# Kernel tuning notes

Measured on AMD Instinct MI355X. Metric: run time of the kernel, lower is better.

## Reference

```python
import jax, jax.numpy as jnp
import numpy as np

B, S, C, M, L = 32, 8192, 64, 16, 4  # batch, seq, n_enc, n_modes, n_layers


def setup_inputs() -> dict:
    key = jax.random.key(0)
    ks = jax.random.split(key, 12)
    scale = 1.0 / (C * M)
    return {
        "input_tensor": jax.random.normal(ks[0], (B, S, 1), dtype=jnp.float32),
        "enc_w": jax.random.normal(ks[1], (C, 1), dtype=jnp.float32) * 0.1,
        "enc_b": jax.random.normal(ks[2], (C,), dtype=jnp.float32) * 0.1,
        "R_re": jax.random.normal(ks[3], (L, C, C, M), dtype=jnp.float32) * scale,
        "R_im": jax.random.normal(ks[4], (L, C, C, M), dtype=jnp.float32) * scale,
        "Wl_w": jax.random.normal(ks[5], (L, C, C), dtype=jnp.float32) * 0.1,
        "Wl_b": jax.random.normal(ks[6], (L, C), dtype=jnp.float32) * 0.1,
        "d1_w": jax.random.normal(ks[7], (C, C), dtype=jnp.float32) * 0.1,
        "d1_b": jax.random.normal(ks[8], (C,), dtype=jnp.float32) * 0.1,
        "d2_w": jax.random.normal(ks[9], (1, C), dtype=jnp.float32) * 0.1,
        "d2_b": jax.random.normal(ks[10], (1,), dtype=jnp.float32) * 0.1,
    }


def reference(input_tensor, enc_w, enc_b, R_re, R_im, Wl_w, Wl_b, d1_w, d1_b, d2_w, d2_b):
    # encoder: Conv1d(1, C, k=1) == per-position dense over channel dim
    h = jnp.einsum('bsi,ci->bsc', input_tensor, enc_w) + enc_b  # [B,S,C]
    n_freq = S // 2 + 1
    for l in range(L):
        x_cs = jnp.swapaxes(h, 1, 2)                 # [B,C,S]
        x_ft = jnp.fft.rfft(x_cs, axis=-1)           # [B,C,n_freq] complex
        Rl = R_re[l] + 1j * R_im[l]                  # [C,C,M]
        y = jnp.einsum('bim,iom->bom', x_ft[:, :, :M], Rl)  # [B,C,M]
        y_full = jnp.concatenate(
            [y, jnp.zeros((B, C, n_freq - M), dtype=y.dtype)], axis=-1)
        spat = jnp.fft.irfft(y_full, n=S, axis=-1)   # [B,C,S] float32
        wout = jnp.einsum('oi,bis->bos', Wl_w[l], x_cs) + Wl_b[l][None, :, None]
        h = jax.nn.gelu(jnp.swapaxes(spat + wout, 1, 2), approximate=False)
    z = jax.nn.gelu(jnp.einsum('bsc,oc->bso', h, d1_w) + d1_b, approximate=False)
    out = jnp.einsum('bso,po->bsp', z, d2_w) + d2_b  # [B,S,1]
    return out
```

## Files before the change

### kernel.cpp

```cpp
#include <hip/hip_runtime.h>
#include <math.h>

#define NB 32
#define NS 8192
#define NC 64
#define NM 16
#define NL 4
#define NM2 32
#define TPOS 128
#define NT (NS/TPOS)
#define PAD 65

typedef float f16v __attribute__((ext_vector_type(16)));
typedef float f8v  __attribute__((ext_vector_type(8)));

static __device__ __forceinline__ f8v zero8() {
    f8v v;
    #pragma unroll
    for (int j = 0; j < 8; ++j) v[j] = 0.0f;
    return v;
}

static __device__ __forceinline__ float gelu_exact(float v) {
    return 0.5f * v * (1.0f + erff(v * 0.7071067811865475f));
}

__global__ void k_table(float* __restrict__ T) {
    int s = blockIdx.x * blockDim.x + threadIdx.x;
    if (s >= NS) return;
    const float w = 6.283185307179586f / (float)NS;
    float* row = T + (size_t)s * NM2;
    #pragma unroll
    for (int m = 0; m < NM; ++m) {
        int idx = (m * s) & (NS - 1);
        float a = w * (float)idx;
        float sv, cv;
        sincosf(a, &sv, &cv);
        row[2*m]   = cv;
        row[2*m+1] = sv;
    }
}

__global__ void k_prep(const float* __restrict__ Ww, const float* __restrict__ d1w,
                       float* __restrict__ Wt, float* __restrict__ d1t) {
    int idx = blockIdx.x * 256 + threadIdx.x;
    if (idx < NL*NC*NC) {
        int l = idx / (NC*NC), r = idx % (NC*NC);
        int i = r / NC, o = r % NC;
        Wt[idx] = Ww[(size_t)l*NC*NC + (size_t)o*NC + i];
    } else if (idx < NL*NC*NC + NC*NC) {
        int r = idx - NL*NC*NC;
        int i = r / NC, o = r % NC;
        d1t[r] = d1w[(size_t)o*NC + i];
    }
}

static __device__ __forceinline__ void dft_phase(
        const float* __restrict__ hs, const float* __restrict__ T,
        float* __restrict__ partial, int b, int tile, int s0,
        int og, int t) {
    int c = t & 63;
    f8v acc = zero8();
    const float* trow = T + (size_t)s0 * NM2 + og * 8;
    #pragma unroll 4
    for (int ss = 0; ss < TPOS; ++ss) {
        float hv = hs[ss * PAD + c];
        f8v tv = *(const f8v*)(trow + (size_t)ss * NM2);
        acc += hv * tv;
    }
    float* pout = partial + (((size_t)b*NT + tile)*NC + c)*NM2 + og*8;
    *(f8v*)pout = acc;
}

__global__ void __launch_bounds__(256) k_enc(const float* __restrict__ x,
                                             const float* __restrict__ ew,
                                             const float* __restrict__ eb,
                                             const float* __restrict__ T,
                                             float* __restrict__ h,
                                             float* __restrict__ partial) {
    __shared__ float hs[TPOS * PAD];
    int tile = blockIdx.x, b = blockIdx.y;
    int t = threadIdx.x;
    int og = __builtin_amdgcn_readfirstlane(t >> 6);
    int p  = t & 63;
    int s0 = tile * TPOS;

    float xA = x[(size_t)b*NS + s0 + p];
    float xB = x[(size_t)b*NS + s0 + p + 64];
    f16v ew16 = *(const f16v*)(ew + og*16);
    f16v eb16 = *(const f16v*)(eb + og*16);
    f16v hA = xA * ew16 + eb16;
    f16v hB = xB * ew16 + eb16;

    *(f16v*)(h + ((size_t)b*NS + s0 + p)*NC + og*16)      = hA;
    *(f16v*)(h + ((size_t)b*NS + s0 + p + 64)*NC + og*16) = hB;

    #pragma unroll
    for (int j = 0; j < 16; ++j) hs[p*PAD + og*16 + j] = hA[j];
    #pragma unroll
    for (int j = 0; j < 16; ++j) hs[(p+64)*PAD + og*16 + j] = hB[j];
    __syncthreads();

    dft_phase(hs, T, partial, b, tile, s0, og, t);
}

__global__ void __launch_bounds__(256) k_mix(const float* __restrict__ partial,
                                             const float* __restrict__ Rre,
                                             const float* __restrict__ Rim,
                                             float* __restrict__ yst, int l) {
    __shared__ float xf[NC * 8];
    int b = blockIdx.x, jg = blockIdx.y, t = threadIdx.x;
    #pragma unroll
    for (int e = 0; e < 2; ++e) {
        int idx = t + 256*e;
        int c = idx >> 3, kk = idx & 7;
        const float* pp = partial + (size_t)b*NT*NC*NM2 + (size_t)c*NM2 + 8*jg + kk;
        float s = 0.f;
        #pragma unroll 8
        for (int tile = 0; tile < NT; ++tile)
            s += pp[(size_t)tile * NC * NM2];
        xf[idx] = s;
    }
    __syncthreads();
    {
        int o = t >> 2, mq = t & 3;
        int m = 4*jg + mq;
        float yre = 0.f, yim = 0.f;
        #pragma unroll 8
        for (int i = 0; i < NC; ++i) {
            float xr = xf[i*8 + 2*mq];
            float xs = xf[i*8 + 2*mq + 1];
            size_t ridx = (((size_t)l*NC + i)*NC + o)*NM + m;
            float rr = Rre[ridx], ri = Rim[ridx];
            yre = fmaf(xr, rr, yre); yre = fmaf(xs, ri, yre);
            yim = fmaf(xr, ri, yim); yim = fmaf(-xs, rr, yim);
        }
        float* yb = yst + (size_t)b*NM2*NC;
        if (m == 0) { yb[o] = yre * (1.0f/NS); yb[NC + o] = 0.f; }
        else {
            yb[(size_t)(2*m)*NC + o]   = yre * (2.0f/NS);
            yb[(size_t)(2*m+1)*NC + o] = -yim * (2.0f/NS);
        }
    }
}

template<bool LAST>
__global__ void __launch_bounds__(256) k_spec(float* __restrict__ h,
                                              const float* __restrict__ T,
                                              const float* __restrict__ yst,
                                              const float* __restrict__ Wt,
                                              const float* __restrict__ Wb,
                                              const float* __restrict__ d1t,
                                              const float* __restrict__ d1b,
                                              const float* __restrict__ d2w,
                                              const float* __restrict__ d2b,
                                              float* __restrict__ partial,
                                              float* __restrict__ outp,
                                              int l) {
    __shared__ float hs[TPOS * PAD];
    __shared__ float red[4 * TPOS];
    int tile = blockIdx.x, b = blockIdx.y;
    int t = threadIdx.x;
    int og = __builtin_amdgcn_readfirstlane(t >> 6);
    int p  = t & 63;
    int s0 = tile * TPOS;

    const float4* hblk = (const float4*)(h + ((size_t)b*NS + s0)*NC);
    float4 ld0 = hblk[t];
    float4 ld1 = hblk[t + 256];
    float4 ld2 = hblk[t + 512];
    float4 ld3 = hblk[t + 768];
    float4 ld4 = hblk[t + 1024];
    float4 ld5 = hblk[t + 1280];
    float4 ld6 = hblk[t + 1536];
    float4 ld7 = hblk[t + 1792];

    const float* Wl = Wt + (size_t)l*NC*NC + og*16;
    const float* bl = Wb + (size_t)l*NC + og*16;
    const float* yb = yst + (size_t)b*NM2*NC + og*16;

    f16v accA = *(const f16v*)bl;
    f16v accB = accA;

    {
        f16v y0 = *(const f16v*)yb;
        accA += y0;
        accB += y0;
        const float w1 = 6.283185307179586f / (float)NS;
        float angA = (float)(s0 + p) * w1;
        float angB = (float)(s0 + p + 64) * w1;
        float cA1, sA1, cB1, sB1;
        sincosf(angA, &sA1, &cA1);
        sincosf(angB, &sB1, &cB1);
        float cmA = cA1, smA = sA1, cmB = cB1, smB = sB1;
        #pragma unroll 1
        for (int m = 1; m < NM; ++m) {
            f16v yc  = *(const f16v*)(yb + (size_t)(2*m)*NC);
            f16v ysv = *(const f16v*)(yb + (size_t)(2*m+1)*NC);
            accA += cmA * yc;  accA += smA * ysv;
            accB += cmB * yc;  accB += smB * ysv;
            float cnA = cmA*cA1 - smA*sA1;
            smA = cmA*sA1 + smA*cA1;  cmA = cnA;
            float cnB = cmB*cB1 - smB*sB1;
            smB = cmB*sB1 + smB*cB1;  cmB = cnB;
        }
    }

    {
        int ss = t >> 4, q4 = (t & 15) * 4;
        float* d;
        d = &hs[ss*PAD + q4];        d[0]=ld0.x; d[1]=ld0.y; d[2]=ld0.z; d[3]=ld0.w;
        d = &hs[(ss+16)*PAD + q4];   d[0]=ld1.x; d[1]=ld1.y; d[2]=ld1.z; d[3]=ld1.w;
        d = &hs[(ss+32)*PAD + q4];   d[0]=ld2.x; d[1]=ld2.y; d[2]=ld2.z; d[3]=ld2.w;
        d = &hs[(ss+48)*PAD + q4];   d[0]=ld3.x; d[1]=ld3.y; d[2]=ld3.z; d[3]=ld3.w;
        d = &hs[(ss+64)*PAD + q4];   d[0]=ld4.x; d[1]=ld4.y; d[2]=ld4.z; d[3]=ld4.w;
        d = &hs[(ss+80)*PAD + q4];   d[0]=ld5.x; d[1]=ld5.y; d[2]=ld5.z; d[3]=ld5.w;
        d = &hs[(ss+96)*PAD + q4];   d[0]=ld6.x; d[1]=ld6.y; d[2]=ld6.z; d[3]=ld6.w;
        d = &hs[(ss+112)*PAD + q4];  d[0]=ld7.x; d[1]=ld7.y; d[2]=ld7.z; d[3]=ld7.w;
    }
    __syncthreads();

    const float* hA = &hs[p * PAD];
    const float* hB = &hs[(p + 64) * PAD];
    #pragma unroll 8
    for (int i = 0; i < NC; ++i) {
        float va = hA[i], vb = hB[i];
        f16v w = *(const f16v*)(Wl + (size_t)i*NC);
        accA += va * w;
        accB += vb * w;
    }

    f16v gA, gB;
    #pragma unroll
    for (int j = 0; j < 16; ++j) gA[j] = gelu_exact(accA[j]);
    #pragma unroll
    for (int j = 0; j < 16; ++j) gB[j] = gelu_exact(accB[j]);
    if (!LAST) {
        *(f16v*)(h + ((size_t)b*NS + s0 + p)*NC + og*16)      = gA;
        *(f16v*)(h + ((size_t)b*NS + s0 + p + 64)*NC + og*16) = gB;
    }

    __syncthreads();
    #pragma unroll
    for (int j = 0; j < 16; ++j) hs[p*PAD + og*16 + j] = gA[j];
    #pragma unroll
    for (int j = 0; j < 16; ++j) hs[(p+64)*PAD + og*16 + j] = gB[j];
    __syncthreads();

    if (!LAST) {
        dft_phase(hs, T, partial, b, tile, s0, og, t);
    } else {
        f16v aA = *(const f16v*)(d1b + og*16);
        f16v aB = aA;
        #pragma unroll 8
        for (int i = 0; i < NC; ++i) {
            float va = hA[i], vb = hB[i];
            f16v w = *(const f16v*)(d1t + (size_t)i*NC + og*16);
            aA += va * w;
            aB += vb * w;
        }
        float resA = 0.f, resB = 0.f;
        #pragma unroll
        for (int j = 0; j < 16; ++j) {
            float dw = d2w[og*16 + j];
            resA = fmaf(gelu_exact(aA[j]), dw, resA);
            resB = fmaf(gelu_exact(aB[j]), dw, resB);
        }
        red[og*TPOS + p]      = resA;
        red[og*TPOS + p + 64] = resB;
        __syncthreads();
        if (t < TPOS) {
            outp[(size_t)b*NS + s0 + t] = d2b[0] + red[t] + red[TPOS + t]
                                        + red[2*TPOS + t] + red[3*TPOS + t];
        }
    }
}

extern "C" void kernel_launch(void* const* d_in, const int* in_sizes, int n_in,
                              void* d_out, int out_size, void* d_ws, size_t ws_size,
                              hipStream_t stream) {
    const float* input = (const float*)d_in[0];
    const float* enc_w = (const float*)d_in[1];
    const float* enc_b = (const float*)d_in[2];
    const float* R_re  = (const float*)d_in[3];
    const float* R_im  = (const float*)d_in[4];
    const float* Wl_w  = (const float*)d_in[5];
    const float* Wl_b  = (const float*)d_in[6];
    const float* d1_w  = (const float*)d_in[7];
    const float* d1_b  = (const float*)d_in[8];
    const float* d2_w  = (const float*)d_in[9];
    const float* d2_b  = (const float*)d_in[10];
    float* out = (float*)d_out;

    float* ws  = (float*)d_ws;
    float* h   = ws;
    float* T   = h   + (size_t)NB*NS*NC;
    float* par = T   + (size_t)NS*NM2;
    float* yst = par + (size_t)NB*NT*NC*NM2;
    float* Wt  = yst + (size_t)NB*NM2*NC;
    float* d1t = Wt  + (size_t)NL*NC*NC;

    hipLaunchKernelGGL(k_table, dim3(NS/256), dim3(256), 0, stream, T);
    hipLaunchKernelGGL(k_prep, dim3((NL*NC*NC + NC*NC + 255)/256), dim3(256), 0,
                       stream, Wl_w, d1_w, Wt, d1t);
    hipLaunchKernelGGL(k_enc, dim3(NT, NB), dim3(256), 0, stream,
                       input, enc_w, enc_b, T, h, par);
    for (int l = 0; l < NL; ++l) {
        hipLaunchKernelGGL(k_mix, dim3(NB, 4), dim3(256), 0, stream,
                           par, R_re, R_im, yst, l);
        if (l < NL - 1) {
            hipLaunchKernelGGL((k_spec<false>), dim3(NT, NB), dim3(256), 0, stream,
                               h, T, yst, Wt, Wl_b, d1t, d1_b, d2_w, d2_b,
                               par, out, l);
        } else {
            hipLaunchKernelGGL((k_spec<true>), dim3(NT, NB), dim3(256), 0, stream,
                               h, T, yst, Wt, Wl_b, d1t, d1_b, d2_w, d2_b,
                               par, out, l);
        }
    }
}
```

Measured before the change: 363.3 us.

## Swizzle LDS tile to channel-major, use fast GELU and hardware sin/cos

Changes the shared-memory tile from a padded position-major layout to a channel-major layout with an XOR swizzle. The goal is to cut bank conflicts and LDS footprint in the DFT and channel-mix loops. Exact erf-based GELU is replaced by an Abramowitz-Stegun polynomial approximation using v_rcp and __expf, and sincosf by hardware v_sin/v_cos plus a rotation for the second position. The reduction buffer is also folded into the reused tile. The approximations cost some accuracy (erf error around 1e-7 absolute, plus hardware trig error).

```diff
diff --git a/kernel.cpp b/kernel.cpp
--- a/kernel.cpp
+++ b/kernel.cpp
@@ -9,7 +9,6 @@
 #define NM2 32
 #define TPOS 128
 #define NT (NS/TPOS)
-#define PAD 65
 
 typedef float f16v __attribute__((ext_vector_type(16)));
 typedef float f8v  __attribute__((ext_vector_type(8)));
@@ -21,8 +20,19 @@
     return v;
 }
 
-static __device__ __forceinline__ float gelu_exact(float v) {
-    return 0.5f * v * (1.0f + erff(v * 0.7071067811865475f));
+static __device__ __forceinline__ float gelu_fast(float v) {
+    float x  = v * 0.7071067811865475f;
+    float ax = fabsf(x);
+    float d  = fmaf(0.3275911f, ax, 1.0f);
+    float t;
+    asm("v_rcp_f32 %0, %1" : "=v"(t) : "v"(d));
+    float p = t * fmaf(t, fmaf(t, fmaf(t, fmaf(t, 1.061405429f, -1.453152027f),
+                                       1.421413741f), -0.284496736f),
+                       0.254829592f);
+    float e = __expf(-ax * ax);
+    float erfv = fmaf(-p, e, 1.0f);
+    erfv = copysignf(erfv, x);
+    return 0.5f * v * (1.0f + erfv);
 }
 
 __global__ void k_table(float* __restrict__ T) {
@@ -60,11 +70,13 @@
         float* __restrict__ partial, int b, int tile, int s0,
         int og, int t) {
     int c = t & 63;
+    int cm = c & 31;
+    const float* hrow = hs + c * TPOS;
     f8v acc = zero8();
     const float* trow = T + (size_t)s0 * NM2 + og * 8;
     #pragma unroll 4
     for (int ss = 0; ss < TPOS; ++ss) {
-        float hv = hs[ss * PAD + c];
+        float hv = hrow[ss ^ cm];
         f8v tv = *(const f8v*)(trow + (size_t)ss * NM2);
         acc += hv * tv;
     }
@@ -78,7 +90,7 @@
                                              const float* __restrict__ T,
                                              float* __restrict__ h,
                                              float* __restrict__ partial) {
-    __shared__ float hs[TPOS * PAD];
+    __shared__ float hs[NC * TPOS];
     int tile = blockIdx.x, b = blockIdx.y;
     int t = threadIdx.x;
     int og = __builtin_amdgcn_readfirstlane(t >> 6);
@@ -96,9 +108,12 @@
     *(f16v*)(h + ((size_t)b*NS + s0 + p + 64)*NC + og*16) = hB;
 
     #pragma unroll
-    for (int j = 0; j < 16; ++j) hs[p*PAD + og*16 + j] = hA[j];
-    #pragma unroll
-    for (int j = 0; j < 16; ++j) hs[(p+64)*PAD + og*16 + j] = hB[j];
+    for (int j = 0; j < 16; ++j) {
+        int c = og*16 + j;
+        int off = p ^ (c & 31);
+        hs[c*TPOS + off]      = hA[j];
+        hs[c*TPOS + off + 64] = hB[j];
+    }
     __syncthreads();
 
     dft_phase(hs, T, partial, b, tile, s0, og, t);
@@ -157,8 +172,7 @@
                                               float* __restrict__ partial,
                                               float* __restrict__ outp,
                                               int l) {
-    __shared__ float hs[TPOS * PAD];
-    __shared__ float red[4 * TPOS];
+    __shared__ float hs[NC * TPOS];
     int tile = blockIdx.x, b = blockIdx.y;
     int t = threadIdx.x;
     int og = __builtin_amdgcn_readfirstlane(t >> 6);
@@ -186,12 +200,14 @@
         f16v y0 = *(const f16v*)yb;
         accA += y0;
         accB += y0;
-        const float w1 = 6.283185307179586f / (float)NS;
-        float angA = (float)(s0 + p) * w1;
-        float angB = (float)(s0 + p + 64) * w1;
-        float cA1, sA1, cB1, sB1;
-        sincosf(angA, &sA1, &cA1);
-        sincosf(angB, &sB1, &cB1);
+        float rev = (float)(s0 + p) * (1.0f / (float)NS);
+        float cA1, sA1;
+        asm("v_cos_f32 %0, %1" : "=v"(cA1) : "v"(rev));
+        asm("v_sin_f32 %0, %1" : "=v"(sA1) : "v"(rev));
+        const float cd = 0.99879545620517239f;
+        const float sd = 0.04906767432741802f;
+        float cB1 = cA1*cd - sA1*sd;
+        float sB1 = sA1*cd + cA1*sd;
         float cmA = cA1, smA = sA1, cmB = cB1, smB = sB1;
         #pragma unroll 1
         for (int m = 1; m < NM; ++m) {
@@ -207,24 +223,27 @@
     }
 
     {
-        int ss = t >> 4, q4 = (t & 15) * 4;
-        float* d;
-        d = &hs[ss*PAD + q4];        d[0]=ld0.x; d[1]=ld0.y; d[2]=ld0.z; d[3]=ld0.w;
-        d = &hs[(ss+16)*PAD + q4];   d[0]=ld1.x; d[1]=ld1.y; d[2]=ld1.z; d[3]=ld1.w;
-        d = &hs[(ss+32)*PAD + q4];   d[0]=ld2.x; d[1]=ld2.y; d[2]=ld2.z; d[3]=ld2.w;
-        d = &hs[(ss+48)*PAD + q4];   d[0]=ld3.x; d[1]=ld3.y; d[2]=ld3.z; d[3]=ld3.w;
-        d = &hs[(ss+64)*PAD + q4];   d[0]=ld4.x; d[1]=ld4.y; d[2]=ld4.z; d[3]=ld4.w;
-        d = &hs[(ss+80)*PAD + q4];   d[0]=ld5.x; d[1]=ld5.y; d[2]=ld5.z; d[3]=ld5.w;
-        d = &hs[(ss+96)*PAD + q4];   d[0]=ld6.x; d[1]=ld6.y; d[2]=ld6.z; d[3]=ld6.w;
-        d = &hs[(ss+112)*PAD + q4];  d[0]=ld7.x; d[1]=ld7.y; d[2]=ld7.z; d[3]=ld7.w;
-    }
-    __syncthreads();
-
-    const float* hA = &hs[p * PAD];
-    const float* hB = &hs[(p + 64) * PAD];
+        float4 lds[8] = {ld0, ld1, ld2, ld3, ld4, ld5, ld6, ld7};
+        #pragma unroll
+        for (int jj = 0; jj < 8; ++jj) {
+            int idx = t + 256*jj;
+            int pos = idx >> 4;
+            int cbase = (idx & 15) * 4;
+            float vals[4] = {lds[jj].x, lds[jj].y, lds[jj].z, lds[jj].w};
+            #pragma unroll
+            for (int j2 = 0; j2 < 4; ++j2) {
+                int c = cbase + j2;
+                hs[c*TPOS + (pos ^ (c & 31))] = vals[j2];
+            }
+        }
+    }
+    __syncthreads();
+
     #pragma unroll 8
     for (int i = 0; i < NC; ++i) {
-        float va = hA[i], vb = hB[i];
+        int off = p ^ (i & 31);
+        float va = hs[i*TPOS + off];
+        float vb = hs[i*TPOS + off + 64];
         f16v w = *(const f16v*)(Wl + (size_t)i*NC);
         accA += va * w;
         accB += vb * w;
@@ -232,9 +251,9 @@
 
     f16v gA, gB;
     #pragma unroll
-    for (int j = 0; j < 16; ++j) gA[j] = gelu_exact(accA[j]);
-    #pragma unroll
-    for (int j = 0; j < 16; ++j) gB[j] = gelu_exact(accB[j]);
+    for (int j = 0; j < 16; ++j) gA[j] = gelu_fast(accA[j]);
+    #pragma unroll
+    for (int j = 0; j < 16; ++j) gB[j] = gelu_fast(accB[j]);
     if (!LAST) {
         *(f16v*)(h + ((size_t)b*NS + s0 + p)*NC + og*16)      = gA;
         *(f16v*)(h + ((size_t)b*NS + s0 + p + 64)*NC + og*16) = gB;
@@ -242,9 +261,12 @@
 
     __syncthreads();
     #pragma unroll
-    for (int j = 0; j < 16; ++j) hs[p*PAD + og*16 + j] = gA[j];
-    #pragma unroll
-    for (int j = 0; j < 16; ++j) hs[(p+64)*PAD + og*16 + j] = gB[j];
+    for (int j = 0; j < 16; ++j) {
+        int c = og*16 + j;
+        int off = p ^ (c & 31);
+        hs[c*TPOS + off]      = gA[j];
+        hs[c*TPOS + off + 64] = gB[j];
+    }
     __syncthreads();
 
     if (!LAST) {
@@ -254,7 +276,9 @@
         f16v aB = aA;
         #pragma unroll 8
         for (int i = 0; i < NC; ++i) {
-            float va = hA[i], vb = hB[i];
+            int off = p ^ (i & 31);
+            float va = hs[i*TPOS + off];
+            float vb = hs[i*TPOS + off + 64];
             f16v w = *(const f16v*)(d1t + (size_t)i*NC + og*16);
             aA += va * w;
             aB += vb * w;
@@ -263,15 +287,16 @@
         #pragma unroll
         for (int j = 0; j < 16; ++j) {
             float dw = d2w[og*16 + j];
-            resA = fmaf(gelu_exact(aA[j]), dw, resA);
-            resB = fmaf(gelu_exact(aB[j]), dw, resB);
-        }
-        red[og*TPOS + p]      = resA;
-        red[og*TPOS + p + 64] = resB;
+            resA = fmaf(gelu_fast(aA[j]), dw, resA);
+            resB = fmaf(gelu_fast(aB[j]), dw, resB);
+        }
+        __syncthreads();
+        hs[og*TPOS + p]      = resA;
+        hs[og*TPOS + p + 64] = resB;
         __syncthreads();
         if (t < TPOS) {
-            outp[(size_t)b*NS + s0 + t] = d2b[0] + red[t] + red[TPOS + t]
-                                        + red[2*TPOS + t] + red[3*TPOS + t];
+            outp[(size_t)b*NS + s0 + t] = d2b[0] + hs[t] + hs[TPOS + t]
+                                        + hs[2*TPOS + t] + hs[3*TPOS + t];
         }
     }
 }
```

Result: slower. 386.2 us (+6.3%).
